# Kernel tuning notes

Hardware: AMD Instinct MI355X
Metric: run time of the kernel (lower is better)

Reference implementation:

```python
import jax, jax.numpy as jnp
import numpy as np

B, T, N, D = 16, 1024, 1024, 256   # batch, query len (hp.max_T), key len (hp.max_N), hp.d
WIN = 64                            # hp.attention_win_size
NEG = jnp.float32(-2**32 + 1)       # padding value used by the TF module


def setup_inputs() -> dict:
    key = jax.random.key(0)
    k1, k2, k3, k4 = jax.random.split(key, 4)
    Q = jax.random.normal(k1, (B, T, D), dtype=jnp.float32)
    K = jax.random.normal(k2, (B, N, D), dtype=jnp.float32)
    V = jax.random.normal(k3, (B, N, D), dtype=jnp.float32)
    prev_max_attentions = jax.random.randint(k4, (B,), 0, N - WIN, dtype=jnp.int64)
    return {"Q": Q, "K": K, "V": V, "prev_max_attentions": prev_max_attentions}


def reference(Q, K, V, prev_max_attentions):
    # scaled scores: [B, T, N]
    A = jnp.einsum("btd,bnd->btn", Q, K) * jax.lax.rsqrt(jnp.float32(D))

    # monotonic window mask (mono_attention=True):
    idx = jnp.arange(N)                              # [N]
    prev = prev_max_attentions[:, None]              # [B, 1]
    masks = (idx < prev) | (idx >= prev + WIN)       # [B, N], True = disallowed
    A = jnp.where(masks[:, None, :], NEG, A)         # broadcast over T (== tf.tile)

    A = jax.nn.softmax(A, axis=-1)                   # [B, T, N]
    max_attentions = jnp.argmax(A, axis=-1).astype(jnp.float32)  # [B, T]

    R = jnp.concatenate([jnp.einsum("btn,bnd->btd", A, V), Q], axis=-1)  # [B, T, 2D]
    alignments = jnp.transpose(A, (0, 2, 1))         # [B, N, T]
    return (R, alignments, max_attentions)
```

## Files before the change

### kernel.cpp

```cpp
#include <hip/hip_runtime.h>


#define BB 16
#define TT 1024
#define NN 1024
#define DD 256
#define WIN 64
#define TBLK 16
#define NT 256

#define R_ELEMS   (16u*1024u*512u)
#define ALN_ELEMS (16u*1024u*1024u)

#define LSTR 132

__global__ __launch_bounds__(256) void zero_nonwin(
    float* __restrict__ aligns, const int* __restrict__ prev_in)
{
    const int b     = blockIdx.x >> 6;
    const int chunk = blockIdx.x & 63;
    const int prev  = prev_in[b];
    float4* base = (float4*)(aligns + (size_t)b * NN * TT);
    const float4 z = make_float4(0.f, 0.f, 0.f, 0.f);
    #pragma unroll
    for (int r = 0; r < 15; ++r) {
        int idx = chunk * 15 + r;
        int n   = idx < prev ? idx : idx + WIN;
        base[(size_t)n * 256 + threadIdx.x] = z;
    }
}

__global__ __launch_bounds__(NT, 4) void attn_v7(
    const float* __restrict__ Q, const float* __restrict__ K,
    const float* __restrict__ V, const int* __restrict__ prev_in,
    float* __restrict__ out)
{
    __shared__ float ks[WIN * LSTR];
    __shared__ float p_lds[TBLK][WIN + 4];

    float* Rout   = out;
    float* aligns = out + R_ELEMS;
    float* maxatt = out + R_ELEMS + ALN_ELEMS;

    const int tid  = threadIdx.x;
    const int lane = tid & 63;
    const int w    = __builtin_amdgcn_readfirstlane(tid >> 6);
    const int b    = blockIdx.x >> 6;
    const int t0   = (blockIdx.x & 63) * TBLK;
    const int prev = prev_in[b];

    const float* qb = Q + ((size_t)b * TT + t0 + 4 * w) * DD;

    float acc[4] = {0.f, 0.f, 0.f, 0.f};
    #pragma unroll
    for (int h = 0; h < 2; ++h) {
        if (h) __syncthreads();
        const float4* Ksrc = (const float4*)(K + ((size_t)b * NN + prev) * DD + h * 128);
        #pragma unroll
        for (int k = 0; k < 8; ++k) {
            int t4 = tid + k * NT;
            int r = t4 >> 5, c = t4 & 31;
            float4 v = Ksrc[(size_t)r * 64 + c];
            *(float4*)&ks[r * LSTR + c * 4] = v;
        }
        __syncthreads();

        const float* qh = qb + h * 128;
        #pragma unroll 8
        for (int d4 = 0; d4 < 32; ++d4) {
            float4 kk = *(const float4*)&ks[lane * LSTR + d4 * 4];
            #pragma unroll
            for (int t = 0; t < 4; ++t) {
                float4 q = ((const float4*)(qh + t * DD))[d4];
                acc[t] = fmaf(q.x, kk.x, fmaf(q.y, kk.y, fmaf(q.z, kk.z, fmaf(q.w, kk.w, acc[t]))));
            }
        }
    }

    #pragma unroll
    for (int t = 0; t < 4; ++t) {
        float v = acc[t] * 0.0625f;

        float m = v;
        #pragma unroll
        for (int off = 32; off; off >>= 1) m = fmaxf(m, __shfl_xor(m, off));

        float e = expf(v - m);
        float s = e;
        #pragma unroll
        for (int off = 32; off; off >>= 1) s += __shfl_xor(s, off);

        p_lds[4 * w + t][lane] = e / s;

        float av = v; int ai = lane;
        #pragma unroll
        for (int off = 32; off; off >>= 1) {
            float ov = __shfl_xor(av, off);
            int   oi = __shfl_xor(ai, off);
            if (ov > av || (ov == av && oi < ai)) { av = ov; ai = oi; }
        }
        if (lane == 0) maxatt[(size_t)b * TT + t0 + 4 * w + t] = (float)(prev + ai);
    }
    __syncthreads();

    {
        const int j = tid >> 2, cg = tid & 3;
        float4 v;
        v.x = p_lds[cg * 4 + 0][j];
        v.y = p_lds[cg * 4 + 1][j];
        v.z = p_lds[cg * 4 + 2][j];
        v.w = p_lds[cg * 4 + 3][j];
        *(float4*)(aligns + ((size_t)b * NN + prev + j) * TT + t0 + cg * 4) = v;
    }

    {
        const float4* V4 = (const float4*)(V + ((size_t)b * NN + prev) * DD);
        float4 o[4];
        #pragma unroll
        for (int t = 0; t < 4; ++t) o[t] = make_float4(0.f, 0.f, 0.f, 0.f);

        #pragma unroll 4
        for (int j4 = 0; j4 < WIN / 4; ++j4) {
            float4 p0 = *(const float4*)&p_lds[4 * w + 0][j4 * 4];
            float4 p1 = *(const float4*)&p_lds[4 * w + 1][j4 * 4];
            float4 p2 = *(const float4*)&p_lds[4 * w + 2][j4 * 4];
            float4 p3 = *(const float4*)&p_lds[4 * w + 3][j4 * 4];
            float4 v0 = V4[(size_t)(j4 * 4 + 0) * 64 + lane];
            float4 v1 = V4[(size_t)(j4 * 4 + 1) * 64 + lane];
            float4 v2 = V4[(size_t)(j4 * 4 + 2) * 64 + lane];
            float4 v3 = V4[(size_t)(j4 * 4 + 3) * 64 + lane];
            #define ACC4(o_, p_) \
                o_.x = fmaf(p_.x, v0.x, fmaf(p_.y, v1.x, fmaf(p_.z, v2.x, fmaf(p_.w, v3.x, o_.x)))); \
                o_.y = fmaf(p_.x, v0.y, fmaf(p_.y, v1.y, fmaf(p_.z, v2.y, fmaf(p_.w, v3.y, o_.y)))); \
                o_.z = fmaf(p_.x, v0.z, fmaf(p_.y, v1.z, fmaf(p_.z, v2.z, fmaf(p_.w, v3.z, o_.z)))); \
                o_.w = fmaf(p_.x, v0.w, fmaf(p_.y, v1.w, fmaf(p_.z, v2.w, fmaf(p_.w, v3.w, o_.w))));
            ACC4(o[0], p0) ACC4(o[1], p1) ACC4(o[2], p2) ACC4(o[3], p3)
            #undef ACC4
        }

        #pragma unroll
        for (int t = 0; t < 4; ++t) {
            float* Rrow = Rout + ((size_t)b * TT + t0 + 4 * w + t) * (2 * DD);
            ((float4*)Rrow)[lane] = o[t];
            ((float4*)(Rrow + DD))[lane] = ((const float4*)(qb + t * DD))[lane];
        }
    }
}

extern "C" void kernel_launch(void* const* d_in, const int* in_sizes, int n_in,
                              void* d_out, int out_size, void* d_ws, size_t ws_size,
                              hipStream_t stream) {
    const float* Q = (const float*)d_in[0];
    const float* K = (const float*)d_in[1];
    const float* V = (const float*)d_in[2];
    const int* prev = (const int*)d_in[3];
    float* out = (float*)d_out;

    zero_nonwin<<<1024, 256, 0, stream>>>(out + R_ELEMS, prev);
    attn_v7<<<BB * TT / TBLK, NT, 0, stream>>>(Q, K, V, prev, out);
}
```

Before: 166.5 us.

## Fuse zero-fill into attention kernel via interleaved blocks and use nontemporal stores

Removes the separate zero_nonwin launch by doubling the grid and having odd blocks zero the out-of-window alignment rows while even blocks do the windowed attention. All large output writes (alignments, R) now use nontemporal stores so streaming output does not pollute cache. This saves a kernel launch and lets zeroing overlap with compute. The cost is more blocks in one grid, and zero blocks may compete for scheduling slots with the compute blocks.

```diff
diff --git a/kernel.cpp b/kernel.cpp
--- a/kernel.cpp
+++ b/kernel.cpp
@@ -14,23 +14,18 @@
 
 #define LSTR 132
 
-__global__ __launch_bounds__(256) void zero_nonwin(
-    float* __restrict__ aligns, const int* __restrict__ prev_in)
-{
-    const int b     = blockIdx.x >> 6;
-    const int chunk = blockIdx.x & 63;
-    const int prev  = prev_in[b];
-    float4* base = (float4*)(aligns + (size_t)b * NN * TT);
-    const float4 z = make_float4(0.f, 0.f, 0.f, 0.f);
-    #pragma unroll
-    for (int r = 0; r < 15; ++r) {
-        int idx = chunk * 15 + r;
-        int n   = idx < prev ? idx : idx + WIN;
-        base[(size_t)n * 256 + threadIdx.x] = z;
-    }
+typedef float nt_f4 __attribute__((ext_vector_type(4)));
+
+__device__ __forceinline__ void nt_store4(void* p, float x, float y, float z, float w) {
+    nt_f4 v = {x, y, z, w};
+    __builtin_nontemporal_store(v, (nt_f4*)p);
+}
+__device__ __forceinline__ void nt_store4v(void* p, const float4& f) {
+    nt_f4 v = {f.x, f.y, f.z, f.w};
+    __builtin_nontemporal_store(v, (nt_f4*)p);
 }
 
-__global__ __launch_bounds__(NT, 4) void attn_v7(
+__global__ __launch_bounds__(NT, 4) void attn_v8(
     const float* __restrict__ Q, const float* __restrict__ K,
     const float* __restrict__ V, const int* __restrict__ prev_in,
     float* __restrict__ out)
@@ -42,11 +37,28 @@
     float* aligns = out + R_ELEMS;
     float* maxatt = out + R_ELEMS + ALN_ELEMS;
 
-    const int tid  = threadIdx.x;
+    const int tid = threadIdx.x;
+
+    if (blockIdx.x & 1) {
+        const int zb    = blockIdx.x >> 1;
+        const int b     = zb >> 6;
+        const int chunk = zb & 63;
+        const int prev  = prev_in[b];
+        float* base = aligns + (size_t)b * NN * TT;
+        #pragma unroll
+        for (int r = 0; r < 15; ++r) {
+            int idx = chunk * 15 + r;
+            int n   = idx < prev ? idx : idx + WIN;
+            nt_store4(base + (size_t)n * TT + tid * 4, 0.f, 0.f, 0.f, 0.f);
+        }
+        return;
+    }
+
     const int lane = tid & 63;
     const int w    = __builtin_amdgcn_readfirstlane(tid >> 6);
-    const int b    = blockIdx.x >> 6;
-    const int t0   = (blockIdx.x & 63) * TBLK;
+    const int ab   = blockIdx.x >> 1;
+    const int b    = ab >> 6;
+    const int t0   = (ab & 63) * TBLK;
     const int prev = prev_in[b];
 
     const float* qb = Q + ((size_t)b * TT + t0 + 4 * w) * DD;
@@ -105,12 +117,9 @@
 
     {
         const int j = tid >> 2, cg = tid & 3;
-        float4 v;
-        v.x = p_lds[cg * 4 + 0][j];
-        v.y = p_lds[cg * 4 + 1][j];
-        v.z = p_lds[cg * 4 + 2][j];
-        v.w = p_lds[cg * 4 + 3][j];
-        *(float4*)(aligns + ((size_t)b * NN + prev + j) * TT + t0 + cg * 4) = v;
+        nt_store4(aligns + ((size_t)b * NN + prev + j) * TT + t0 + cg * 4,
+                  p_lds[cg * 4 + 0][j], p_lds[cg * 4 + 1][j],
+                  p_lds[cg * 4 + 2][j], p_lds[cg * 4 + 3][j]);
     }
 
     {
@@ -141,8 +150,9 @@
         #pragma unroll
         for (int t = 0; t < 4; ++t) {
             float* Rrow = Rout + ((size_t)b * TT + t0 + 4 * w + t) * (2 * DD);
-            ((float4*)Rrow)[lane] = o[t];
-            ((float4*)(Rrow + DD))[lane] = ((const float4*)(qb + t * DD))[lane];
+            nt_store4v(Rrow + lane * 4, o[t]);
+            float4 qv = ((const float4*)(qb + t * DD))[lane];
+            nt_store4v(Rrow + DD + lane * 4, qv);
         }
     }
 }
@@ -156,6 +166,5 @@
     const int* prev = (const int*)d_in[3];
     float* out = (float*)d_out;
 
-    zero_nonwin<<<1024, 256, 0, stream>>>(out + R_ELEMS, prev);
-    attn_v7<<<BB * TT / TBLK, NT, 0, stream>>>(Q, K, V, prev, out);
+    attn_v8<<<2 * (BB * TT / TBLK), NT, 0, stream>>>(Q, K, V, prev, out);
 }
```

After: 193.0 us. 15.9% more time.
